# Kernel tuning notes

Measured on AMD Instinct MI355X. Metric: run time of the kernel, lower is better.

Reference implementation:

```python
import jax, jax.numpy as jnp
import numpy as np

N, M, D_IN, H1, D, OUT_C = 2048, 128, 352, 512, 256, 13


def _lin_bn_relu(x, w, b, g, be):
    # 1x1 conv == linear over last dim; BN (eval) folded to per-channel affine (g, be)
    return jax.nn.relu(g * (x @ w.T + b) + be)


def _encode(x, wA, bA, gA, beA, wB, bB, gB, beB):
    return _lin_bn_relu(_lin_bn_relu(x, wA, bA, gA, beA), wB, bB, gB, beB)


def setup_inputs() -> dict:
    key = jax.random.key(0)
    ks = iter(jax.random.split(key, 64))

    def wgt(shape, s=0.05):
        return (jax.random.normal(next(ks), shape, jnp.float32) * s)

    def gamma(c):
        return 1.0 + 0.05 * jax.random.normal(next(ks), (c,), jnp.float32)

    inp = {}
    inp['ext_fea'] = jax.random.normal(next(ks), (N, D_IN), jnp.float32)
    inp['lab_fea'] = jax.random.normal(next(ks), (M, D_IN), jnp.float32)
    # convs1: 352->512->256, each Conv1d(1x1)+BN+ReLU
    inp.update(w1a=wgt((H1, D_IN)), b1a=wgt((H1,)), g1a=gamma(H1), be1a=wgt((H1,)))
    inp.update(w1b=wgt((D, H1)), b1b=wgt((D,)), g1b=gamma(D), be1b=wgt((D,)))
    # convs2: same shapes
    inp.update(w2a=wgt((H1, D_IN)), b2a=wgt((H1,)), g2a=gamma(H1), be2a=wgt((H1,)))
    inp.update(w2b=wgt((D, H1)), b2b=wgt((D,)), g2b=gamma(D), be2b=wgt((D,)))
    # wei_conv SharedMLP [256,32,64,256]: three Conv2d(1x1)+BN+ReLU
    inp.update(mw1=wgt((32, D)), mb1=wgt((32,)), mg1=gamma(32), mbe1=wgt((32,)))
    inp.update(mw2=wgt((64, 32)), mb2=wgt((64,)), mg2=gamma(64), mbe2=wgt((64,)))
    inp.update(mw3=wgt((D, 64)), mb3=wgt((D,)), mg3=gamma(D), mbe3=wgt((D,)))
    # fc
    inp.update(fcw=wgt((OUT_C, D)), fcb=wgt((OUT_C,)))
    return inp


def reference(ext_fea, lab_fea,
              w1a, b1a, g1a, be1a, w1b, b1b, g1b, be1b,
              w2a, b2a, g2a, be2a, w2b, b2b, g2b, be2b,
              mw1, mb1, mg1, mbe1, mw2, mb2, mg2, mbe2, mw3, mb3, mg3, mbe3,
              fcw, fcb):
    A = _encode(ext_fea, w1a, b1a, g1a, be1a, w1b, b1b, g1b, be1b)   # [N, 256]
    B = _encode(lab_fea, w2a, b2a, g2a, be2a, w2b, b2b, g2b, be2b)   # [M, 256]
    diff = A[:, None, :] - B[None, :, :]                             # [N, M, 256]
    h = _lin_bn_relu(diff, mw1, mb1, mg1, mbe1)                      # [N, M, 32]
    h = _lin_bn_relu(h, mw2, mb2, mg2, mbe2)                         # [N, M, 64]
    wei = _lin_bn_relu(h, mw3, mb3, mg3, mbe3)                       # [N, M, 256]
    # torch softmax over dim=-1 of [1,256,N,M] == over M == axis 1 here
    wei = jax.nn.softmax(wei, axis=1)
    att = jnp.sum(wei * diff, axis=1)                                # [N, 256]
    return att @ fcw.T + fcb                                         # [N, 13]
```

## Files before the change

kernel.cpp:

```cpp
#include <hip/hip_runtime.h>
#include <stdint.h>


typedef __attribute__((ext_vector_type(4))) float float4_t;
typedef __attribute__((ext_vector_type(4))) float f32x4;
typedef __attribute__((ext_vector_type(8))) short bf16x8;
typedef __attribute__((ext_vector_type(8))) unsigned short ushort8_t;
typedef unsigned short ushort_t;

__device__ __forceinline__ unsigned short f2b(float f) {
  union { float f; unsigned int i; } v; v.f = f;
  unsigned int x = v.i;
  return (unsigned short)((x + 0x7FFFu + ((x >> 16) & 1u)) >> 16);
}

__global__ __launch_bounds__(256) void cvt_bf16(
    const float* __restrict__ s0, const float* __restrict__ s1,
    const float* __restrict__ s2, const float* __restrict__ s3,
    const float* __restrict__ s4, const float* __restrict__ s5,
    const float* __restrict__ s6, const float* __restrict__ s7,
    ushort_t* __restrict__ d0, ushort_t* __restrict__ d1,
    ushort_t* __restrict__ d2, ushort_t* __restrict__ d3,
    ushort_t* __restrict__ d4, ushort_t* __restrict__ d5,
    ushort_t* __restrict__ d6, ushort_t* __restrict__ d7)
{
  int i = blockIdx.x * 256 + threadIdx.x;
  const float* s; ushort_t* d; int j;
  if      (i < 90112)  { s = s0; d = d0; j = i; }
  else if (i < 95744)  { s = s1; d = d1; j = i - 90112; }
  else if (i < 118272) { s = s2; d = d2; j = i - 95744; }
  else if (i < 134656) { s = s3; d = d3; j = i - 118272; }
  else if (i < 157184) { s = s4; d = d4; j = i - 134656; }
  else if (i < 173568) { s = s5; d = d5; j = i - 157184; }
  else if (i < 173824) { s = s6; d = d6; j = i - 173568; }
  else                 { s = s7; d = d7; j = i - 173824; }
  float4_t v0 = *(const float4_t*)&s[(size_t)j * 8];
  float4_t v1 = *(const float4_t*)&s[(size_t)j * 8 + 4];
  ushort8_t u;
  #pragma unroll
  for (int e = 0; e < 4; ++e) { u[e] = f2b(v0[e]); u[4 + e] = f2b(v1[e]); }
  *(ushort8_t*)&d[(size_t)j * 8] = u;
}

template<int OUT_BF16>
__global__ __launch_bounds__(256) void enc_mfma(
    const ushort_t* __restrict__ XA, const ushort_t* __restrict__ WA,
    const float* __restrict__ bA, const float* __restrict__ gA, const float* __restrict__ beA,
    void* __restrict__ YA,
    const ushort_t* __restrict__ XB, const ushort_t* __restrict__ WB,
    const float* __restrict__ bB, const float* __restrict__ gB, const float* __restrict__ beB,
    void* __restrict__ YB, float* __restrict__ YBT,
    int J, int K, int nbxA)
{
  __shared__ ushort_t Xs[64][40];
  __shared__ ushort_t Ws[64][40];
  const int bx = blockIdx.x, by = blockIdx.y;
  const ushort_t* X; const ushort_t* W;
  const float *bb, *gg, *bev; void* Y; int i0, isB;
  if (bx < nbxA) { X = XA; W = WA; bb = bA; gg = gA; bev = beA; Y = YA; i0 = bx * 64; isB = 0; }
  else           { X = XB; W = WB; bb = bB; gg = gB; bev = beB; Y = YB; i0 = (bx - nbxA) * 64; isB = 1; }
  const int j0 = by * 64;
  const int tid = threadIdx.x, w = tid >> 6, lane = tid & 63, lg = lane >> 4, lr = lane & 15;
  const int sr = tid >> 2, sk = (tid & 3) * 8;

  f32x4 acc[4];
  #pragma unroll
  for (int mt = 0; mt < 4; ++mt) acc[mt] = f32x4{0.f, 0.f, 0.f, 0.f};

  ushort8_t xv = *(const ushort8_t*)&X[(size_t)(i0 + sr) * K + sk];
  ushort8_t wv = *(const ushort8_t*)&W[(size_t)(j0 + sr) * K + sk];
  for (int kt = 0; kt < K; kt += 32) {
    __syncthreads();
    *(ushort8_t*)&Xs[sr][sk] = xv;
    *(ushort8_t*)&Ws[sr][sk] = wv;
    __syncthreads();
    if (kt + 32 < K) {
      xv = *(const ushort8_t*)&X[(size_t)(i0 + sr) * K + kt + 32 + sk];
      wv = *(const ushort8_t*)&W[(size_t)(j0 + sr) * K + kt + 32 + sk];
    }
    bf16x8 bfrag = *(const bf16x8*)&Ws[w * 16 + lr][lg * 8];
    #pragma unroll
    for (int mt = 0; mt < 4; ++mt) {
      bf16x8 af = *(const bf16x8*)&Xs[mt * 16 + lr][lg * 8];
      acc[mt] = __builtin_amdgcn_mfma_f32_16x16x32_bf16(af, bfrag, acc[mt], 0, 0, 0);
    }
  }
  const int c = j0 + w * 16 + lr;
  const float g = gg[c], bv = bb[c], ev = bev[c];
  #pragma unroll
  for (int mt = 0; mt < 4; ++mt)
    #pragma unroll
    for (int r = 0; r < 4; ++r) {
      const int row = i0 + mt * 16 + 4 * lg + r;
      float t = fmaxf(g * (acc[mt][r] + bv) + ev, 0.f);
      if (OUT_BF16) ((ushort_t*)Y)[(size_t)row * J + c] = f2b(t);
      else {
        ((float*)Y)[(size_t)row * J + c] = t;
        if (isB && YBT) YBT[(size_t)c * 128 + row] = t;
      }
    }
}

__global__ __launch_bounds__(256) void proj32(
    const float* __restrict__ Aenc, const float* __restrict__ Benc,
    const float* __restrict__ mw1, const float* __restrict__ mb1,
    const float* __restrict__ mg1, const float* __restrict__ mbe1,
    float* __restrict__ PA2, float* __restrict__ PB2, int nbxA)
{
  const int tid = threadIdx.x, bx = blockIdx.x;
  const float* X; float* P; int n0, wb;
  if (bx < nbxA) { X = Aenc; P = PA2; n0 = bx * 8; wb = 1; }
  else           { X = Benc; P = PB2; n0 = (bx - nbxA) * 8; wb = 0; }
  const int r = tid >> 5, k = tid & 31;
  const int n = n0 + r;
  const float* xp = &X[(size_t)n * 256];
  const float* wp = &mw1[k * 256];
  float s = 0.f;
  #pragma unroll 8
  for (int q = 0; q < 256; q += 4) {
    float4_t xv = *(const float4_t*)&xp[q];
    float4_t wv = *(const float4_t*)&wp[q];
    #pragma unroll
    for (int e = 0; e < 4; ++e) s = fmaf(xv[e], wv[e], s);
  }
  P[(size_t)n * 32 + k] = wb ? (mg1[k] * (s + mb1[k]) + mbe1[k]) : (mg1[k] * s);
}

__global__ __launch_bounds__(256, 2) void main_attn(
    const float* __restrict__ PA2, const float* __restrict__ PB2,
    const float* __restrict__ A, const float* __restrict__ BmT,
    const ushort_t* __restrict__ mw2b, const float* __restrict__ mb2,
    const float* __restrict__ mg2, const float* __restrict__ mbe2,
    const ushort_t* __restrict__ mw3b, const float* __restrict__ mb3,
    const float* __restrict__ mg3, const float* __restrict__ mbe3,
    const float* __restrict__ fcw, const float* __restrict__ fcb,
    float* __restrict__ outp)
{
  __shared__ __align__(16) char smem[28672];
  ushort_t* h1s = (ushort_t*)smem;
  ushort_t* h2s = (ushort_t*)(smem + 10240);
  float* attL = (float*)smem;
  float* part = (float*)(smem + 1024);

  const int tid = threadIdx.x;
  const int w = tid >> 6, lane = tid & 63, lg = lane >> 4, lr = lane & 15;
  const int n = blockIdx.x;
  const float LOG2E = 1.4426950408889634f;

  {
    const int m = tid >> 1, half = tid & 1;
    const float* pa = &PA2[(size_t)n * 32 + half * 16];
    const float* pb = &PB2[(size_t)m * 32 + half * 16];
    #pragma unroll
    for (int q = 0; q < 2; ++q) {
      float4_t a0 = *(const float4_t*)&pa[q * 8];
      float4_t a1 = *(const float4_t*)&pa[q * 8 + 4];
      float4_t b0 = *(const float4_t*)&pb[q * 8];
      float4_t b1 = *(const float4_t*)&pb[q * 8 + 4];
      ushort8_t u;
      #pragma unroll
      for (int e = 0; e < 4; ++e) {
        u[e]     = f2b(fmaxf(a0[e] - b0[e], 0.f));
        u[4 + e] = f2b(fmaxf(a1[e] - b1[e], 0.f));
      }
      *(ushort8_t*)&h1s[m * 40 + half * 16 + q * 8] = u;
    }
  }
  __syncthreads();

  {
    f32x4 acc1[2][4];
    #pragma unroll
    for (int mt = 0; mt < 2; ++mt)
      #pragma unroll
      for (int jt = 0; jt < 4; ++jt) acc1[mt][jt] = f32x4{0.f, 0.f, 0.f, 0.f};
    bf16x8 a1[2], b1[4];
    #pragma unroll
    for (int mt = 0; mt < 2; ++mt)
      a1[mt] = *(const bf16x8*)&h1s[(w * 32 + mt * 16 + lr) * 40 + lg * 8];
    #pragma unroll
    for (int jt = 0; jt < 4; ++jt)
      b1[jt] = *(const bf16x8*)&mw2b[(jt * 16 + lr) * 32 + lg * 8];
    #pragma unroll
    for (int mt = 0; mt < 2; ++mt)
      #pragma unroll
      for (int jt = 0; jt < 4; ++jt)
        acc1[mt][jt] = __builtin_amdgcn_mfma_f32_16x16x32_bf16(a1[mt], b1[jt], acc1[mt][jt], 0, 0, 0);
    #pragma unroll
    for (int jt = 0; jt < 4; ++jt) {
      const int j = jt * 16 + lr;
      const float g = mg2[j], bv = mb2[j], ev = mbe2[j];
      #pragma unroll
      for (int mt = 0; mt < 2; ++mt)
        #pragma unroll
        for (int r = 0; r < 4; ++r)
          h2s[(w * 32 + mt * 16 + 4 * lg + r) * 72 + jt * 16 + lr] =
              f2b(fmaxf(g * (acc1[mt][jt][r] + bv) + ev, 0.f));
    }
  }
  __syncthreads();

  float mxv[4], smv[4], wbv[4];
  #pragma unroll
  for (int cp = 0; cp < 2; ++cp) {
    f32x4 acc[8][2];
    #pragma unroll
    for (int mt = 0; mt < 8; ++mt) {
      acc[mt][0] = f32x4{0.f, 0.f, 0.f, 0.f};
      acc[mt][1] = f32x4{0.f, 0.f, 0.f, 0.f};
    }
    #pragma unroll
    for (int ks = 0; ks < 2; ++ks) {
      bf16x8 bfr[2];
      #pragma unroll
      for (int q = 0; q < 2; ++q) {
        const int c = w * 64 + (cp * 2 + q) * 16 + lr;
        bfr[q] = *(const bf16x8*)&mw3b[(size_t)c * 64 + ks * 32 + lg * 8];
      }
      #pragma unroll
      for (int mt = 0; mt < 8; ++mt) {
        bf16x8 af = *(const bf16x8*)&h2s[(mt * 16 + lr) * 72 + ks * 32 + lg * 8];
        acc[mt][0] = __builtin_amdgcn_mfma_f32_16x16x32_bf16(af, bfr[0], acc[mt][0], 0, 0, 0);
        acc[mt][1] = __builtin_amdgcn_mfma_f32_16x16x32_bf16(af, bfr[1], acc[mt][1], 0, 0, 0);
      }
    }
    #pragma unroll
    for (int q = 0; q < 2; ++q) {
      const int ct = cp * 2 + q;
      const int c = w * 64 + ct * 16 + lr;
      const float g = mg3[c], bv = mb3[c], ev = mbe3[c];
      const float gs = g * LOG2E;
      const float cs = (g * bv + ev) * LOG2E;
      float mx = 0.f;
      #pragma unroll
      for (int mt = 0; mt < 8; ++mt)
        #pragma unroll
        for (int r = 0; r < 4; ++r) {
          float t = fmaxf(fmaf(gs, acc[mt][q][r], cs), 0.f);
          acc[mt][q][r] = t;
          mx = fmaxf(mx, t);
        }
      float sm = 0.f, wb = 0.f;
      #pragma unroll
      for (int mt = 0; mt < 8; ++mt) {
        float4_t bv4 = *(const float4_t*)&BmT[(size_t)c * 128 + mt * 16 + 4 * lg];
        #pragma unroll
        for (int r = 0; r < 4; ++r) {
          float p = exp2f(acc[mt][q][r] - mx);
          sm += p;
          wb = fmaf(p, bv4[r], wb);
        }
      }
      mxv[ct] = mx; smv[ct] = sm; wbv[ct] = wb;
    }
  }
  #pragma unroll
  for (int st = 16; st <= 32; st <<= 1) {
    #pragma unroll
    for (int ct = 0; ct < 4; ++ct) {
      float omx = __shfl_xor(mxv[ct], st, 64);
      float osm = __shfl_xor(smv[ct], st, 64);
      float owb = __shfl_xor(wbv[ct], st, 64);
      float nm = fmaxf(mxv[ct], omx);
      float e0 = exp2f(mxv[ct] - nm), e1 = exp2f(omx - nm);
      smv[ct] = smv[ct] * e0 + osm * e1;
      wbv[ct] = wbv[ct] * e0 + owb * e1;
      mxv[ct] = nm;
    }
  }

  __syncthreads();
  if (lg == 0) {
    #pragma unroll
    for (int ct = 0; ct < 4; ++ct) {
      const int c = w * 64 + ct * 16 + lr;
      attL[c] = A[(size_t)n * 256 + c] - wbv[ct] / fmaxf(smv[ct], 1e-30f);
    }
  }
  __syncthreads();

  {
    const int o = tid >> 4, gp = tid & 15;
    if (o < 13) {
      float s = 0.f;
      #pragma unroll
      for (int i = 0; i < 4; ++i) {
        float4_t av = *(const float4_t*)&attL[gp * 16 + i * 4];
        float4_t wv = *(const float4_t*)&fcw[(size_t)o * 256 + gp * 16 + i * 4];
        #pragma unroll
        for (int e = 0; e < 4; ++e) s = fmaf(av[e], wv[e], s);
      }
      part[o * 16 + gp] = s;
    }
  }
  __syncthreads();
  if (tid < 13) {
    float s = fcb[tid];
    #pragma unroll
    for (int gp = 0; gp < 16; ++gp) s += part[tid * 16 + gp];
    outp[(size_t)n * 13 + tid] = s;
  }
}

extern "C" void kernel_launch(void* const* d_in, const int* in_sizes, int n_in,
                              void* d_out, int out_size, void* d_ws, size_t ws_size,
                              hipStream_t stream)
{
  const float* ext = (const float*)d_in[0];
  const float* lab = (const float*)d_in[1];
  const float* w1a = (const float*)d_in[2];
  const float* b1a = (const float*)d_in[3];
  const float* g1a = (const float*)d_in[4];
  const float* be1a= (const float*)d_in[5];
  const float* w1b = (const float*)d_in[6];
  const float* b1b = (const float*)d_in[7];
  const float* g1b = (const float*)d_in[8];
  const float* be1b= (const float*)d_in[9];
  const float* w2a = (const float*)d_in[10];
  const float* b2a = (const float*)d_in[11];
  const float* g2a = (const float*)d_in[12];
  const float* be2a= (const float*)d_in[13];
  const float* w2b = (const float*)d_in[14];
  const float* b2b = (const float*)d_in[15];
  const float* g2b = (const float*)d_in[16];
  const float* be2b= (const float*)d_in[17];
  const float* mw1 = (const float*)d_in[18];
  const float* mb1 = (const float*)d_in[19];
  const float* mg1 = (const float*)d_in[20];
  const float* mbe1= (const float*)d_in[21];
  const float* mw2 = (const float*)d_in[22];
  const float* mb2 = (const float*)d_in[23];
  const float* mg2 = (const float*)d_in[24];
  const float* mbe2= (const float*)d_in[25];
  const float* mw3 = (const float*)d_in[26];
  const float* mb3 = (const float*)d_in[27];
  const float* mg3 = (const float*)d_in[28];
  const float* mbe3= (const float*)d_in[29];
  const float* fcw = (const float*)d_in[30];
  const float* fcb = (const float*)d_in[31];

  char* ws = (char*)d_ws;
  ushort_t* Y1ab = (ushort_t*)(ws);
  float*    PA2  = (float*)(ws);
  float*    PB2  = (float*)(ws + 262144);
  float*    Aenc = (float*)(ws + (2u << 20));
  ushort_t* extb = (ushort_t*)(ws + (2u << 20));
  char* b5 = ws + (4u << 20);
  ushort_t* w1ab = (ushort_t*)(b5);
  ushort_t* w1bb = (ushort_t*)(b5 + 360448);
  ushort_t* w2ab = (ushort_t*)(b5 + 622592);
  ushort_t* w2bb = (ushort_t*)(b5 + 983040);
  ushort_t* mw2b = (ushort_t*)(b5 + 1245184);
  ushort_t* mw3b = (ushort_t*)(b5 + 1249280);
  ushort_t* labb = (ushort_t*)(b5 + 1282048);
  ushort_t* Y1bb = (ushort_t*)(b5 + 1372160);
  float*    Benc = (float*)(b5 + 1503232);
  float*    BencT= (float*)(b5 + 1634304);

  cvt_bf16<<<687, 256, 0, stream>>>(ext, lab, w1a, w1b, w2a, w2b, mw2, mw3,
                                    extb, labb, w1ab, w1bb, w2ab, w2bb, mw2b, mw3b);
  enc_mfma<1><<<dim3(34, 8), 256, 0, stream>>>(
      extb, w1ab, b1a, g1a, be1a, (void*)Y1ab,
      labb, w2ab, b2a, g2a, be2a, (void*)Y1bb, (float*)nullptr, 512, 352, 32);
  enc_mfma<0><<<dim3(34, 4), 256, 0, stream>>>(
      Y1ab, w1bb, b1b, g1b, be1b, (void*)Aenc,
      Y1bb, w2bb, b2b, g2b, be2b, (void*)Benc, BencT, 256, 512, 32);
  proj32<<<272, 256, 0, stream>>>(Aenc, Benc, mw1, mb1, mg1, mbe1, PA2, PB2, 256);
  main_attn<<<2048, 256, 0, stream>>>(PA2, PB2, Aenc, BencT,
                                      mw2b, mb2, mg2, mbe2, mw3b, mb3, mg3, mbe3,
                                      fcw, fcb, (float*)d_out);
}
```

Baseline: 99.83 us.

## Fuse bf16 conversion into loads, drop max-subtraction in softmax, load h1 directly

```diff
diff --git a/kernel.cpp b/kernel.cpp
--- a/kernel.cpp
+++ b/kernel.cpp
@@ -14,40 +14,27 @@
   return (unsigned short)((x + 0x7FFFu + ((x >> 16) & 1u)) >> 16);
 }
 
-__global__ __launch_bounds__(256) void cvt_bf16(
-    const float* __restrict__ s0, const float* __restrict__ s1,
-    const float* __restrict__ s2, const float* __restrict__ s3,
-    const float* __restrict__ s4, const float* __restrict__ s5,
-    const float* __restrict__ s6, const float* __restrict__ s7,
-    ushort_t* __restrict__ d0, ushort_t* __restrict__ d1,
-    ushort_t* __restrict__ d2, ushort_t* __restrict__ d3,
-    ushort_t* __restrict__ d4, ushort_t* __restrict__ d5,
-    ushort_t* __restrict__ d6, ushort_t* __restrict__ d7)
-{
-  int i = blockIdx.x * 256 + threadIdx.x;
-  const float* s; ushort_t* d; int j;
-  if      (i < 90112)  { s = s0; d = d0; j = i; }
-  else if (i < 95744)  { s = s1; d = d1; j = i - 90112; }
-  else if (i < 118272) { s = s2; d = d2; j = i - 95744; }
-  else if (i < 134656) { s = s3; d = d3; j = i - 118272; }
-  else if (i < 157184) { s = s4; d = d4; j = i - 134656; }
-  else if (i < 173568) { s = s5; d = d5; j = i - 157184; }
-  else if (i < 173824) { s = s6; d = d6; j = i - 173568; }
-  else                 { s = s7; d = d7; j = i - 173824; }
-  float4_t v0 = *(const float4_t*)&s[(size_t)j * 8];
-  float4_t v1 = *(const float4_t*)&s[(size_t)j * 8 + 4];
-  ushort8_t u;
-  #pragma unroll
-  for (int e = 0; e < 4; ++e) { u[e] = f2b(v0[e]); u[4 + e] = f2b(v1[e]); }
-  *(ushort8_t*)&d[(size_t)j * 8] = u;
-}
-
-template<int OUT_BF16>
+template<int ISBF>
+__device__ __forceinline__ ushort8_t ld8(const void* base, size_t idx) {
+  if constexpr (ISBF) {
+    return *(const ushort8_t*)((const ushort_t*)base + idx);
+  } else {
+    const float* p = (const float*)base + idx;
+    float4_t v0 = *(const float4_t*)p;
+    float4_t v1 = *(const float4_t*)(p + 4);
+    ushort8_t u;
+    #pragma unroll
+    for (int e = 0; e < 4; ++e) { u[e] = f2b(v0[e]); u[4 + e] = f2b(v1[e]); }
+    return u;
+  }
+}
+
+template<int XBF, int WBF, int OUT_BF16>
 __global__ __launch_bounds__(256) void enc_mfma(
-    const ushort_t* __restrict__ XA, const ushort_t* __restrict__ WA,
+    const void* __restrict__ XA, const void* __restrict__ WA,
     const float* __restrict__ bA, const float* __restrict__ gA, const float* __restrict__ beA,
     void* __restrict__ YA,
-    const ushort_t* __restrict__ XB, const ushort_t* __restrict__ WB,
+    const void* __restrict__ XB, const void* __restrict__ WB,
     const float* __restrict__ bB, const float* __restrict__ gB, const float* __restrict__ beB,
     void* __restrict__ YB, float* __restrict__ YBT,
     int J, int K, int nbxA)
@@ -55,7 +42,7 @@
   __shared__ ushort_t Xs[64][40];
   __shared__ ushort_t Ws[64][40];
   const int bx = blockIdx.x, by = blockIdx.y;
-  const ushort_t* X; const ushort_t* W;
+  const void* X; const void* W;
   const float *bb, *gg, *bev; void* Y; int i0, isB;
   if (bx < nbxA) { X = XA; W = WA; bb = bA; gg = gA; bev = beA; Y = YA; i0 = bx * 64; isB = 0; }
   else           { X = XB; W = WB; bb = bB; gg = gB; bev = beB; Y = YB; i0 = (bx - nbxA) * 64; isB = 1; }
@@ -67,16 +54,16 @@
   #pragma unroll
   for (int mt = 0; mt < 4; ++mt) acc[mt] = f32x4{0.f, 0.f, 0.f, 0.f};
 
-  ushort8_t xv = *(const ushort8_t*)&X[(size_t)(i0 + sr) * K + sk];
-  ushort8_t wv = *(const ushort8_t*)&W[(size_t)(j0 + sr) * K + sk];
+  ushort8_t xv = ld8<XBF>(X, (size_t)(i0 + sr) * K + sk);
+  ushort8_t wv = ld8<WBF>(W, (size_t)(j0 + sr) * K + sk);
   for (int kt = 0; kt < K; kt += 32) {
     __syncthreads();
     *(ushort8_t*)&Xs[sr][sk] = xv;
     *(ushort8_t*)&Ws[sr][sk] = wv;
     __syncthreads();
     if (kt + 32 < K) {
-      xv = *(const ushort8_t*)&X[(size_t)(i0 + sr) * K + kt + 32 + sk];
-      wv = *(const ushort8_t*)&W[(size_t)(j0 + sr) * K + kt + 32 + sk];
+      xv = ld8<XBF>(X, (size_t)(i0 + sr) * K + kt + 32 + sk);
+      wv = ld8<WBF>(W, (size_t)(j0 + sr) * K + kt + 32 + sk);
     }
     bf16x8 bfrag = *(const bf16x8*)&Ws[w * 16 + lr][lg * 8];
     #pragma unroll
@@ -105,9 +92,24 @@
     const float* __restrict__ Aenc, const float* __restrict__ Benc,
     const float* __restrict__ mw1, const float* __restrict__ mb1,
     const float* __restrict__ mg1, const float* __restrict__ mbe1,
-    float* __restrict__ PA2, float* __restrict__ PB2, int nbxA)
+    float* __restrict__ PA2, float* __restrict__ PB2, int nbxA,
+    const float* __restrict__ mw2, const float* __restrict__ mw3,
+    ushort_t* __restrict__ mw2b, ushort_t* __restrict__ mw3b)
 {
   const int tid = threadIdx.x, bx = blockIdx.x;
+  if (bx >= nbxA + 16) {
+    const int g = (bx - nbxA - 16) * 256 + tid;
+    const float* s; ushort_t* d; int j;
+    if (g < 256) { s = mw2; d = mw2b; j = g; }
+    else         { s = mw3; d = mw3b; j = g - 256; }
+    float4_t v0 = *(const float4_t*)&s[(size_t)j * 8];
+    float4_t v1 = *(const float4_t*)&s[(size_t)j * 8 + 4];
+    ushort8_t u;
+    #pragma unroll
+    for (int e = 0; e < 4; ++e) { u[e] = f2b(v0[e]); u[4 + e] = f2b(v1[e]); }
+    *(ushort8_t*)&d[(size_t)j * 8] = u;
+    return;
+  }
   const float* X; float* P; int n0, wb;
   if (bx < nbxA) { X = Aenc; P = PA2; n0 = bx * 8; wb = 1; }
   else           { X = Benc; P = PB2; n0 = (bx - nbxA) * 8; wb = 0; }
@@ -136,9 +138,8 @@
     const float* __restrict__ fcw, const float* __restrict__ fcb,
     float* __restrict__ outp)
 {
-  __shared__ __align__(16) char smem[28672];
-  ushort_t* h1s = (ushort_t*)smem;
-  ushort_t* h2s = (ushort_t*)(smem + 10240);
+  __shared__ __align__(16) char smem[18432];
+  ushort_t* h2s = (ushort_t*)smem;
   float* attL = (float*)smem;
   float* part = (float*)(smem + 1024);
 
@@ -148,36 +149,31 @@
   const float LOG2E = 1.4426950408889634f;
 
   {
-    const int m = tid >> 1, half = tid & 1;
-    const float* pa = &PA2[(size_t)n * 32 + half * 16];
-    const float* pb = &PB2[(size_t)m * 32 + half * 16];
-    #pragma unroll
-    for (int q = 0; q < 2; ++q) {
-      float4_t a0 = *(const float4_t*)&pa[q * 8];
-      float4_t a1 = *(const float4_t*)&pa[q * 8 + 4];
-      float4_t b0 = *(const float4_t*)&pb[q * 8];
-      float4_t b1 = *(const float4_t*)&pb[q * 8 + 4];
-      ushort8_t u;
-      #pragma unroll
-      for (int e = 0; e < 4; ++e) {
-        u[e]     = f2b(fmaxf(a0[e] - b0[e], 0.f));
-        u[4 + e] = f2b(fmaxf(a1[e] - b1[e], 0.f));
-      }
-      *(ushort8_t*)&h1s[m * 40 + half * 16 + q * 8] = u;
-    }
-  }
-  __syncthreads();
-
-  {
     f32x4 acc1[2][4];
     #pragma unroll
     for (int mt = 0; mt < 2; ++mt)
       #pragma unroll
       for (int jt = 0; jt < 4; ++jt) acc1[mt][jt] = f32x4{0.f, 0.f, 0.f, 0.f};
     bf16x8 a1[2], b1[4];
-    #pragma unroll
-    for (int mt = 0; mt < 2; ++mt)
-      a1[mt] = *(const bf16x8*)&h1s[(w * 32 + mt * 16 + lr) * 40 + lg * 8];
+    {
+      const float* pa = &PA2[(size_t)n * 32 + lg * 8];
+      float4_t pa0 = *(const float4_t*)pa;
+      float4_t pa1 = *(const float4_t*)(pa + 4);
+      #pragma unroll
+      for (int mt = 0; mt < 2; ++mt) {
+        const int m = w * 32 + mt * 16 + lr;
+        const float* pb = &PB2[(size_t)m * 32 + lg * 8];
+        float4_t pb0 = *(const float4_t*)pb;
+        float4_t pb1 = *(const float4_t*)(pb + 4);
+        bf16x8 u;
+        #pragma unroll
+        for (int e = 0; e < 4; ++e) {
+          u[e]     = (short)f2b(fmaxf(pa0[e] - pb0[e], 0.f));
+          u[4 + e] = (short)f2b(fmaxf(pa1[e] - pb1[e], 0.f));
+        }
+        a1[mt] = u;
+      }
+    }
     #pragma unroll
     for (int jt = 0; jt < 4; ++jt)
       b1[jt] = *(const bf16x8*)&mw2b[(jt * 16 + lr) * 32 + lg * 8];
@@ -200,7 +196,7 @@
   }
   __syncthreads();
 
-  float mxv[4], smv[4], wbv[4];
+  float smv[4], wbv[4];
   #pragma unroll
   for (int cp = 0; cp < 2; ++cp) {
     f32x4 acc[8][2];
@@ -231,41 +227,29 @@
       const float g = mg3[c], bv = mb3[c], ev = mbe3[c];
       const float gs = g * LOG2E;
       const float cs = (g * bv + ev) * LOG2E;
-      float mx = 0.f;
-      #pragma unroll
-      for (int mt = 0; mt < 8; ++mt)
-        #pragma unroll
-        for (int r = 0; r < 4; ++r) {
-          float t = fmaxf(fmaf(gs, acc[mt][q][r], cs), 0.f);
-          acc[mt][q][r] = t;
-          mx = fmaxf(mx, t);
-        }
-      float sm = 0.f, wb = 0.f;
+      f32x4 sm4 = f32x4{0.f, 0.f, 0.f, 0.f};
+      f32x4 wb4 = f32x4{0.f, 0.f, 0.f, 0.f};
       #pragma unroll
       for (int mt = 0; mt < 8; ++mt) {
         float4_t bv4 = *(const float4_t*)&BmT[(size_t)c * 128 + mt * 16 + 4 * lg];
         #pragma unroll
         for (int r = 0; r < 4; ++r) {
-          float p = exp2f(acc[mt][q][r] - mx);
-          sm += p;
-          wb = fmaf(p, bv4[r], wb);
+          float t = fmaf(gs, acc[mt][q][r], cs);
+          float p = exp2f(__builtin_amdgcn_fmed3f(t, 0.f, 80.f));
+          sm4[r] += p;
+          wb4[r] = fmaf(p, bv4[r], wb4[r]);
         }
       }
-      mxv[ct] = mx; smv[ct] = sm; wbv[ct] = wb;
+      smv[ct] = (sm4[0] + sm4[1]) + (sm4[2] + sm4[3]);
+      wbv[ct] = (wb4[0] + wb4[1]) + (wb4[2] + wb4[3]);
     }
   }
   #pragma unroll
   for (int st = 16; st <= 32; st <<= 1) {
     #pragma unroll
     for (int ct = 0; ct < 4; ++ct) {
-      float omx = __shfl_xor(mxv[ct], st, 64);
-      float osm = __shfl_xor(smv[ct], st, 64);
-      float owb = __shfl_xor(wbv[ct], st, 64);
-      float nm = fmaxf(mxv[ct], omx);
-      float e0 = exp2f(mxv[ct] - nm), e1 = exp2f(omx - nm);
-      smv[ct] = smv[ct] * e0 + osm * e1;
-      wbv[ct] = wbv[ct] * e0 + owb * e1;
-      mxv[ct] = nm;
+      smv[ct] += __shfl_xor(smv[ct], st, 64);
+      wbv[ct] += __shfl_xor(wbv[ct], st, 64);
     }
   }
 
@@ -274,7 +258,7 @@
     #pragma unroll
     for (int ct = 0; ct < 4; ++ct) {
       const int c = w * 64 + ct * 16 + lr;
-      attL[c] = A[(size_t)n * 256 + c] - wbv[ct] / fmaxf(smv[ct], 1e-30f);
+      attL[c] = A[(size_t)n * 256 + c] - wbv[ct] / smv[ct];
     }
   }
   __syncthreads();
@@ -344,28 +328,23 @@
   float*    PA2  = (float*)(ws);
   float*    PB2  = (float*)(ws + 262144);
   float*    Aenc = (float*)(ws + (2u << 20));
-  ushort_t* extb = (ushort_t*)(ws + (2u << 20));
   char* b5 = ws + (4u << 20);
-  ushort_t* w1ab = (ushort_t*)(b5);
-  ushort_t* w1bb = (ushort_t*)(b5 + 360448);
-  ushort_t* w2ab = (ushort_t*)(b5 + 622592);
-  ushort_t* w2bb = (ushort_t*)(b5 + 983040);
-  ushort_t* mw2b = (ushort_t*)(b5 + 1245184);
-  ushort_t* mw3b = (ushort_t*)(b5 + 1249280);
-  ushort_t* labb = (ushort_t*)(b5 + 1282048);
-  ushort_t* Y1bb = (ushort_t*)(b5 + 1372160);
-  float*    Benc = (float*)(b5 + 1503232);
-  float*    BencT= (float*)(b5 + 1634304);
-
-  cvt_bf16<<<687, 256, 0, stream>>>(ext, lab, w1a, w1b, w2a, w2b, mw2, mw3,
-                                    extb, labb, w1ab, w1bb, w2ab, w2bb, mw2b, mw3b);
-  enc_mfma<1><<<dim3(34, 8), 256, 0, stream>>>(
-      extb, w1ab, b1a, g1a, be1a, (void*)Y1ab,
-      labb, w2ab, b2a, g2a, be2a, (void*)Y1bb, (float*)nullptr, 512, 352, 32);
-  enc_mfma<0><<<dim3(34, 4), 256, 0, stream>>>(
-      Y1ab, w1bb, b1b, g1b, be1b, (void*)Aenc,
-      Y1bb, w2bb, b2b, g2b, be2b, (void*)Benc, BencT, 256, 512, 32);
-  proj32<<<272, 256, 0, stream>>>(Aenc, Benc, mw1, mb1, mg1, mbe1, PA2, PB2, 256);
+  ushort_t* mw2b = (ushort_t*)(b5);
+  ushort_t* mw3b = (ushort_t*)(b5 + 4096);
+  ushort_t* Y1bb = (ushort_t*)(b5 + 36864);
+  float*    Benc = (float*)(b5 + 167936);
+  float*    BencT= (float*)(b5 + 299008);
+
+  enc_mfma<0, 0, 1><<<dim3(34, 8), 256, 0, stream>>>(
+      (const void*)ext, (const void*)w1a, b1a, g1a, be1a, (void*)Y1ab,
+      (const void*)lab, (const void*)w2a, b2a, g2a, be2a, (void*)Y1bb,
+      (float*)nullptr, 512, 352, 32);
+  enc_mfma<1, 0, 0><<<dim3(34, 4), 256, 0, stream>>>(
+      (const void*)Y1ab, (const void*)w1b, b1b, g1b, be1b, (void*)Aenc,
+      (const void*)Y1bb, (const void*)w2b, b2b, g2b, be2b, (void*)Benc,
+      BencT, 256, 512, 32);
+  proj32<<<281, 256, 0, stream>>>(Aenc, Benc, mw1, mb1, mg1, mbe1, PA2, PB2, 256,
+                                  mw2, mw3, mw2b, mw3b);
   main_attn<<<2048, 256, 0, stream>>>(PA2, PB2, Aenc, BencT,
                                       mw2b, mb2, mg2, mbe2, mw3b, mb3, mg3, mbe3,
                                       fcw, fcb, (float*)d_out);
```

Result: no change. 98.90 us (-0.9%).
